# Kernel tuning notes

Hardware: AMD Instinct MI355X
Metric: run time of the kernel (lower is better)

## Reference

```python
import jax, jax.numpy as jnp
import numpy as np
from jax import lax

K = 3
STRIDE = 1
PAD = 1
DIL = 1


def _rrsvm(x, s):
    # x: [B, C, H, W], s: [C, K, K]
    B, C, H, W = x.shape
    # im2col: [B, C*K*K, Ho, Wo], channel-major patch ordering -> reshape (C, K*K)
    patches = lax.conv_general_dilated_patches(
        x, (K, K), (STRIDE, STRIDE), [(PAD, PAD), (PAD, PAD)],
        rhs_dilation=(DIL, DIL))
    Ho, Wo = patches.shape[2], patches.shape[3]
    p = patches.reshape(B, C, K * K, Ho, Wo)
    # descending sort of each window's values (rank pooling order)
    order = jnp.argsort(-p, axis=2)                      # [B, C, K*K, Ho, Wo]
    sorted_p = jnp.take_along_axis(p, order, axis=2)
    # learned per-rank weights, per channel
    out = jnp.einsum('bckhw,ck->bchw', sorted_p, s.reshape(C, K * K))
    indices = jnp.transpose(order, (0, 1, 3, 4, 2))      # [B, C, Ho, Wo, K*K]
    return out, indices


def setup_inputs() -> dict:
    key = jax.random.key(0)
    k1, k2 = jax.random.split(key)
    B, C, H, W = 16, 128, 56, 56
    x = jax.random.normal(k1, (B, C, H, W), dtype=jnp.float32)
    # module inits s to 1/(C*K*K); use random positive weights for a non-degenerate test
    s = jax.random.uniform(k2, (C, K, K), dtype=jnp.float32) / (K * K)
    return {"x": x, "s": s}


def reference(x, s):
    return _rrsvm(x, s)
```

## Files before the change

kernel.cpp:

```cpp
#include <hip/hip_runtime.h>


#define B_ 16
#define C_ 128
#define H_ 56
#define W_ 56
#define NOUT (B_*C_*H_*W_)
#define BLK 256

#define CE(i, j) do {                                   \
    float vi = v[(i)], vj = v[(j)];                     \
    float ii = id[(i)], ij = id[(j)];                   \
    bool sw = vj > vi;                                  \
    v[(i)]  = sw ? vj : vi;  v[(j)]  = sw ? vi : vj;    \
    id[(i)] = sw ? ij : ii;  id[(j)] = sw ? ii : ij;    \
} while (0)

__global__ __launch_bounds__(BLK) void rrsvm_kernel(
    const float* __restrict__ x, const float* __restrict__ s,
    float* __restrict__ out, float* __restrict__ idxout)
{
    __shared__ float lds[BLK * 9];

    const int tid = threadIdx.x;
    const int gid = blockIdx.x * BLK + tid;

    const int w  = gid % W_;
    const int t  = gid / W_;
    const int h  = t % H_;
    const int bc = t / H_;
    const int c  = bc % C_;

    const float* xp = x + gid;
    float v[9];
    float id[9];
    #pragma unroll
    for (int dy = 0; dy < 3; ++dy) {
        #pragma unroll
        for (int dx = 0; dx < 3; ++dx) {
            const int k  = dy * 3 + dx;
            const int hh = h + dy - 1;
            const int ww = w + dx - 1;
            float val = 0.0f;
            if ((unsigned)hh < (unsigned)H_ && (unsigned)ww < (unsigned)W_)
                val = xp[(dy - 1) * W_ + (dx - 1)];
            v[k]  = val;
            id[k] = (float)k;
        }
    }

    #pragma unroll
    for (int rnd = 0; rnd < 9; ++rnd) {
        if ((rnd & 1) == 0) {
            CE(0, 1); CE(2, 3); CE(4, 5); CE(6, 7);
        } else {
            CE(1, 2); CE(3, 4); CE(5, 6); CE(7, 8);
        }
    }

    const float* sp = s + c * 9;
    float acc = 0.0f;
    #pragma unroll
    for (int r = 0; r < 9; ++r)
        acc = fmaf(v[r], sp[r], acc);
    out[gid] = acc;

    #pragma unroll
    for (int r = 0; r < 9; ++r)
        lds[tid * 9 + r] = id[r];
    __syncthreads();

    float4* dst = (float4*)(idxout + (size_t)blockIdx.x * (BLK * 9));
    const float4* src = (const float4*)lds;
    dst[tid]       = src[tid];
    dst[tid + 256] = src[tid + 256];
    if (tid < 64)
        dst[tid + 512] = src[tid + 512];
}

extern "C" void kernel_launch(void* const* d_in, const int* in_sizes, int n_in,
                              void* d_out, int out_size, void* d_ws, size_t ws_size,
                              hipStream_t stream) {
    const float* x = (const float*)d_in[0];
    const float* s = (const float*)d_in[1];
    float* out    = (float*)d_out;
    float* idxout = out + NOUT;

    const int nblocks = NOUT / BLK;
    rrsvm_kernel<<<nblocks, BLK, 0, stream>>>(x, s, out, idxout);
}
```

Before: 284.4 us.

## Process two adjacent pixels per thread with shared taps and nontemporal index stores

After: 279.3 us. No clear change (-1.8%).

```diff
diff --git a/kernel.cpp b/kernel.cpp
--- a/kernel.cpp
+++ b/kernel.cpp
@@ -5,77 +5,114 @@
 #define C_ 128
 #define H_ 56
 #define W_ 56
-#define NOUT (B_*C_*H_*W_)
+#define NPIX (B_*C_*H_*W_)
 #define BLK 256
+#define PXB (BLK * 2)
 
-#define CE(i, j) do {                                   \
-    float vi = v[(i)], vj = v[(j)];                     \
-    float ii = id[(i)], ij = id[(j)];                   \
-    bool sw = vj > vi;                                  \
-    v[(i)]  = sw ? vj : vi;  v[(j)]  = sw ? vi : vj;    \
-    id[(i)] = sw ? ij : ii;  id[(j)] = sw ? ii : ij;    \
-} while (0)
+typedef float v4f __attribute__((ext_vector_type(4)));
+
+__device__ __forceinline__ void sort9(float v[9], float id[9]) {
+    #pragma unroll
+    for (int rnd = 0; rnd < 9; ++rnd) {
+        #pragma unroll
+        for (int i = (rnd & 1); i + 1 < 9; i += 2) {
+            float vi = v[i], vj = v[i + 1];
+            float ii = id[i], ij = id[i + 1];
+            bool sw = vj > vi;
+            v[i]      = sw ? vj : vi;  v[i + 1]  = sw ? vi : vj;
+            id[i]     = sw ? ij : ii;  id[i + 1] = sw ? ii : ij;
+        }
+    }
+}
 
 __global__ __launch_bounds__(BLK) void rrsvm_kernel(
     const float* __restrict__ x, const float* __restrict__ s,
     float* __restrict__ out, float* __restrict__ idxout)
 {
-    __shared__ float lds[BLK * 9];
+    __shared__ float lds[PXB * 9];
 
     const int tid = threadIdx.x;
-    const int gid = blockIdx.x * BLK + tid;
+    const int pix = (blockIdx.x * BLK + tid) * 2;
+    const int w0  = pix % W_;
+    const int t   = pix / W_;
+    const int h   = t % H_;
+    const int bc  = t / H_;
+    const int c   = bc & (C_ - 1);
 
-    const int w  = gid % W_;
-    const int t  = gid / W_;
-    const int h  = t % H_;
-    const int bc = t / H_;
-    const int c  = bc % C_;
+    const float* sp = s + c * 9;
+    float sw9[9];
+    #pragma unroll
+    for (int r = 0; r < 9; ++r) sw9[r] = sp[r];
 
-    const float* xp = x + gid;
-    float v[9];
-    float id[9];
-    #pragma unroll
-    for (int dy = 0; dy < 3; ++dy) {
+    const float* img = x + (size_t)bc * (H_ * W_);
+    const int r0 = (h > 0)       ? h - 1  : 0;
+    const int r2 = (h < H_ - 1)  ? h + 1  : H_ - 1;
+    const int c0 = (w0 > 0)      ? w0 - 1 : 0;
+    const int c3 = (w0 < W_ - 2) ? w0 + 2 : W_ - 1;
+    const float* p0 = img + r0 * W_;
+    const float* p1 = img + h  * W_;
+    const float* p2 = img + r2 * W_;
+
+    float tap[3][4];
+    tap[0][0] = p0[c0]; tap[0][1] = p0[w0]; tap[0][2] = p0[w0 + 1]; tap[0][3] = p0[c3];
+    tap[1][0] = p1[c0]; tap[1][1] = p1[w0]; tap[1][2] = p1[w0 + 1]; tap[1][3] = p1[c3];
+    tap[2][0] = p2[c0]; tap[2][1] = p2[w0]; tap[2][2] = p2[w0 + 1]; tap[2][3] = p2[c3];
+
+    const bool rv0 = (h > 0), rv2 = (h < H_ - 1);
+    const bool cvL = (w0 > 0), cvR = (w0 < W_ - 2);
+    tap[0][0] = (rv0 && cvL) ? tap[0][0] : 0.0f;
+    tap[0][1] = rv0          ? tap[0][1] : 0.0f;
+    tap[0][2] = rv0          ? tap[0][2] : 0.0f;
+    tap[0][3] = (rv0 && cvR) ? tap[0][3] : 0.0f;
+    tap[1][0] = cvL          ? tap[1][0] : 0.0f;
+    tap[1][3] = cvR          ? tap[1][3] : 0.0f;
+    tap[2][0] = (rv2 && cvL) ? tap[2][0] : 0.0f;
+    tap[2][1] = rv2          ? tap[2][1] : 0.0f;
+    tap[2][2] = rv2          ? tap[2][2] : 0.0f;
+    tap[2][3] = (rv2 && cvR) ? tap[2][3] : 0.0f;
+
+    float* lbase = lds + tid * 18;
+    float2 o;
+
+    {
+        float v[9]  = { tap[0][0], tap[0][1], tap[0][2],
+                        tap[1][0], tap[1][1], tap[1][2],
+                        tap[2][0], tap[2][1], tap[2][2] };
+        float id[9] = { 0, 1, 2, 3, 4, 5, 6, 7, 8 };
+        sort9(v, id);
+        float acc = 0.0f;
         #pragma unroll
-        for (int dx = 0; dx < 3; ++dx) {
-            const int k  = dy * 3 + dx;
-            const int hh = h + dy - 1;
-            const int ww = w + dx - 1;
-            float val = 0.0f;
-            if ((unsigned)hh < (unsigned)H_ && (unsigned)ww < (unsigned)W_)
-                val = xp[(dy - 1) * W_ + (dx - 1)];
-            v[k]  = val;
-            id[k] = (float)k;
-        }
+        for (int r = 0; r < 9; ++r) acc = fmaf(v[r], sw9[r], acc);
+        o.x = acc;
+        #pragma unroll
+        for (int r = 0; r < 9; ++r) lbase[r] = id[r];
+    }
+    {
+        float v[9]  = { tap[0][1], tap[0][2], tap[0][3],
+                        tap[1][1], tap[1][2], tap[1][3],
+                        tap[2][1], tap[2][2], tap[2][3] };
+        float id[9] = { 0, 1, 2, 3, 4, 5, 6, 7, 8 };
+        sort9(v, id);
+        float acc = 0.0f;
+        #pragma unroll
+        for (int r = 0; r < 9; ++r) acc = fmaf(v[r], sw9[r], acc);
+        o.y = acc;
+        #pragma unroll
+        for (int r = 0; r < 9; ++r) lbase[9 + r] = id[r];
     }
 
-    #pragma unroll
-    for (int rnd = 0; rnd < 9; ++rnd) {
-        if ((rnd & 1) == 0) {
-            CE(0, 1); CE(2, 3); CE(4, 5); CE(6, 7);
-        } else {
-            CE(1, 2); CE(3, 4); CE(5, 6); CE(7, 8);
-        }
-    }
+    *(float2*)(out + pix) = o;
 
-    const float* sp = s + c * 9;
-    float acc = 0.0f;
-    #pragma unroll
-    for (int r = 0; r < 9; ++r)
-        acc = fmaf(v[r], sp[r], acc);
-    out[gid] = acc;
-
-    #pragma unroll
-    for (int r = 0; r < 9; ++r)
-        lds[tid * 9 + r] = id[r];
     __syncthreads();
 
-    float4* dst = (float4*)(idxout + (size_t)blockIdx.x * (BLK * 9));
-    const float4* src = (const float4*)lds;
-    dst[tid]       = src[tid];
-    dst[tid + 256] = src[tid + 256];
-    if (tid < 64)
-        dst[tid + 512] = src[tid + 512];
+    v4f* dst = (v4f*)(idxout + (size_t)blockIdx.x * (PXB * 9));
+    const v4f* src = (const v4f*)lds;
+    __builtin_nontemporal_store(src[tid],        dst + tid);
+    __builtin_nontemporal_store(src[tid + 256],  dst + tid + 256);
+    __builtin_nontemporal_store(src[tid + 512],  dst + tid + 512);
+    __builtin_nontemporal_store(src[tid + 768],  dst + tid + 768);
+    if (tid < 128)
+        __builtin_nontemporal_store(src[tid + 1024], dst + tid + 1024);
 }
 
 extern "C" void kernel_launch(void* const* d_in, const int* in_sizes, int n_in,
@@ -84,8 +121,8 @@
     const float* x = (const float*)d_in[0];
     const float* s = (const float*)d_in[1];
     float* out    = (float*)d_out;
-    float* idxout = out + NOUT;
+    float* idxout = out + NPIX;
 
-    const int nblocks = NOUT / BLK;
+    const int nblocks = NPIX / PXB;
     rrsvm_kernel<<<nblocks, BLK, 0, stream>>>(x, s, out, idxout);
 }
```
